# Kernel tuning notes

Hardware: AMD Instinct MI355X
Metric: run time of the kernel (lower is better)

## Reference

```python
import jax, jax.numpy as jnp
import numpy as np

N = 100000   # nodes
E = 1600000  # directed edges
F_IN = 100
H = 256
N_LABELS = 19
BN_EPS = 1e-5


def setup_inputs() -> dict:
    key = jax.random.key(0)
    ks = jax.random.split(key, 12)
    p = lambda k, shape, s=0.05: jax.random.normal(k, shape, dtype=jnp.float32) * s
    return {
        "x": jax.random.normal(ks[0], (N, F_IN), dtype=jnp.float32),
        "edge_index": jax.random.randint(ks[1], (2, E), 0, N, dtype=jnp.int32),
        "W1": p(ks[2], (F_IN, F_IN)), "b1": jnp.zeros((F_IN,), jnp.float32),
        "W2": p(ks[3], (F_IN, F_IN)), "b2": jnp.zeros((F_IN,), jnp.float32),
        "W3": p(ks[4], (F_IN, H)),   "b3": jnp.zeros((H,), jnp.float32),
        "fc1_W": p(ks[5], (H, H)),   "fc1_b": jnp.zeros((H,), jnp.float32),
        "fc2a_W": p(ks[6], (H, 128)), "fc2a_b": jnp.zeros((128,), jnp.float32),
        "bn_gamma": jnp.ones((128,), jnp.float32), "bn_beta": jnp.zeros((128,), jnp.float32),
        "fc2b_W": p(ks[7], (128, N_LABELS)), "fc2b_b": jnp.zeros((N_LABELS,), jnp.float32),
    }


def _gcn_conv(x, W, b, src, dst, dinv):
    """PyG GCNConv with add_self_loops + symmetric normalization.
    out[dst] += dinv[src]*dinv[dst] * (x @ W)[src], plus self-loop term, plus bias.
    """
    n = x.shape[0]
    xw = x @ W  # [N, out]
    norm = dinv[src] * dinv[dst]  # [E]
    agg = jax.ops.segment_sum(xw[src] * norm[:, None], dst, num_segments=n)
    agg = agg + xw * (dinv * dinv)[:, None]  # self loops (i -> i)
    return agg + b


def reference(x, edge_index, W1, b1, W2, b2, W3, b3, fc1_W, fc1_b,
              fc2a_W, fc2a_b, bn_gamma, bn_beta, fc2b_W, fc2b_b):
    src, dst = edge_index[0], edge_index[1]
    n = x.shape[0]
    # degree of augmented graph (A + I), computed on targets (sum aggregation)
    deg = jax.ops.segment_sum(jnp.ones((src.shape[0],), x.dtype), dst, num_segments=n) + 1.0
    dinv = jax.lax.rsqrt(deg)

    h = jnp.clip(x, -0.4, 0.4)
    h = jax.nn.relu(_gcn_conv(h, W1, b1, src, dst, dinv))
    h = jax.nn.relu(_gcn_conv(h, W2, b2, src, dst, dinv))
    h = jax.nn.relu(_gcn_conv(h, W3, b3, src, dst, dinv))
    h = jax.nn.relu(h @ fc1_W + fc1_b)
    # fc2: Linear -> BatchNorm1d (train mode, batch stats) -> ReLU -> Linear
    h = h @ fc2a_W + fc2a_b
    mu = jnp.mean(h, axis=0)
    var = jnp.mean(jnp.square(h - mu), axis=0)  # biased var, as torch BN uses
    h = (h - mu) * jax.lax.rsqrt(var + BN_EPS) * bn_gamma + bn_beta
    h = jax.nn.relu(h)
    logits = h @ fc2b_W + fc2b_b
    return jax.nn.log_softmax(logits, axis=1)
```

## Files before the change

kernel.cpp:

```cpp
#include <hip/hip_runtime.h>
#include <hip/hip_bf16.h>

#define N_NODES 100000
#define N_EDGES 1600000
#define F_IN_DIM 100
#define F_IN_PAD 104
#define H_DIM 256
#define BN_DIM 128
#define N_LABELS 19
#define BN_EPS 1e-5f
#define M_PAD 100096

#define BUCKET_SHIFT 8
#define NB 391
#define EPB 4096
#define PB 391

#define PACK_TOTAL 145728
#define CLIP_TOTAL (N_NODES * 13)

typedef __attribute__((ext_vector_type(8))) short bf16x8;
typedef __attribute__((ext_vector_type(4))) short s16x4;
typedef __attribute__((ext_vector_type(4))) float f32x4;

static __device__ inline short f2bf(float f) {
    __hip_bfloat16 h = __float2bfloat16(f);
    return *(short*)&h;
}
static __device__ inline float bf2f(short s) {
    unsigned u = ((unsigned)(unsigned short)s) << 16;
    return __builtin_bit_cast(float, u);
}

#define GLOAD_LDS16(g, l) \
    __builtin_amdgcn_global_load_lds((__attribute__((address_space(1))) const unsigned int*)(g), \
                                     (__attribute__((address_space(3))) unsigned int*)(l), 16, 0, 0)

__global__ __launch_bounds__(256) void part_hist_kernel(const int* __restrict__ dst,
                                                        int* __restrict__ part_hist, int E)
{
    __shared__ int h[NB];
    int tid = threadIdx.x;
    for (int i = tid; i < NB; i += 256) h[i] = 0;
    __syncthreads();
    int base = blockIdx.x * EPB;
    int end = min(base + EPB, E);
    for (int e = base + tid; e < end; e += 256)
        atomicAdd(&h[dst[e] >> BUCKET_SHIFT], 1);
    __syncthreads();
    for (int i = tid; i < NB; i += 256) part_hist[blockIdx.x * NB + i] = h[i];
}

__global__ __launch_bounds__(512) void bucket_total_kernel(const int* __restrict__ part_hist,
                                                           int* __restrict__ bucket_total)
{
    __shared__ int ls[512];
    int b = blockIdx.x;
    int s = 0;
    for (int p = threadIdx.x; p < PB; p += 512) s += part_hist[p * NB + b];
    ls[threadIdx.x] = s;
    __syncthreads();
    for (int off = 256; off > 0; off >>= 1) {
        if (threadIdx.x < off) ls[threadIdx.x] += ls[threadIdx.x + off];
        __syncthreads();
    }
    if (threadIdx.x == 0) bucket_total[b] = ls[0];
}

__global__ __launch_bounds__(512) void bucket_scan_kernel(const int* __restrict__ bucket_total,
                                                          int* __restrict__ bucket_base)
{
    __shared__ int ls[512];
    int tid = threadIdx.x;
    ls[tid] = (tid < NB) ? bucket_total[tid] : 0;
    __syncthreads();
    for (int off = 1; off < 512; off <<= 1) {
        int v = ls[tid];
        int add = (tid >= off) ? ls[tid - off] : 0;
        __syncthreads();
        ls[tid] = v + add;
        __syncthreads();
    }
    if (tid < NB) bucket_base[tid] = (tid > 0) ? ls[tid - 1] : 0;
    if (tid == 0) bucket_base[NB] = ls[NB - 1];
}

__global__ __launch_bounds__(512) void part_offset_kernel(int* __restrict__ part_hist,
                                                          const int* __restrict__ bucket_base)
{
    __shared__ int ls[512];
    int b = blockIdx.x;
    int tid = threadIdx.x;
    int v = (tid < PB) ? part_hist[tid * NB + b] : 0;
    ls[tid] = v;
    __syncthreads();
    for (int off = 1; off < 512; off <<= 1) {
        int x = ls[tid];
        int add = (tid >= off) ? ls[tid - off] : 0;
        __syncthreads();
        ls[tid] = x + add;
        __syncthreads();
    }
    if (tid < PB) part_hist[tid * NB + b] = bucket_base[b] + ((tid > 0) ? ls[tid - 1] : 0);
}

__global__ __launch_bounds__(256) void partition_kernel(const int* __restrict__ src,
                                                        const int* __restrict__ dst,
                                                        const int* __restrict__ part_hist,
                                                        int* __restrict__ ep, int E)
{
    __shared__ int cur[NB];
    int tid = threadIdx.x;
    for (int i = tid; i < NB; i += 256) cur[i] = part_hist[blockIdx.x * NB + i];
    __syncthreads();
    int base = blockIdx.x * EPB;
    int end = min(base + EPB, E);
    for (int e = base + tid; e < end; e += 256) {
        int d = dst[e];
        int s = src[e];
        int pos = atomicAdd(&cur[d >> BUCKET_SHIFT], 1);
        ep[pos] = (s << 8) | (d & 255);
    }
}

__global__ __launch_bounds__(256) void bucket_csr_kernel(const int* __restrict__ ep,
                                                         const int* __restrict__ bucket_base,
                                                         int* __restrict__ row_start,
                                                         float* __restrict__ dinv,
                                                         int* __restrict__ src_sorted, int N, int E)
{
    __shared__ int h[256], sc[256], cur[256];
    int b = blockIdx.x;
    int tid = threadIdx.x;
    int e0 = bucket_base[b], e1 = bucket_base[b + 1];
    int node0 = b << BUCKET_SHIFT;
    int nn = min(256, N - node0);

    h[tid] = 0;
    __syncthreads();
    for (int e = e0 + tid; e < e1; e += 256)
        atomicAdd(&h[ep[e] & 255], 1);
    __syncthreads();

    sc[tid] = h[tid];
    __syncthreads();
    for (int off = 1; off < 256; off <<= 1) {
        int v = sc[tid];
        int add = (tid >= off) ? sc[tid - off] : 0;
        __syncthreads();
        sc[tid] = v + add;
        __syncthreads();
    }
    int excl = e0 + ((tid > 0) ? sc[tid - 1] : 0);
    if (tid < nn) {
        row_start[node0 + tid] = excl;
        dinv[node0 + tid] = rsqrtf((float)h[tid] + 1.0f);
    }
    cur[tid] = excl;
    __syncthreads();
    for (int e = e0 + tid; e < e1; e += 256) {
        int p = ep[e];
        int pos = atomicAdd(&cur[p & 255], 1);
        src_sorted[pos] = ((unsigned)p) >> 8;
    }
    if (b == 0 && tid == 0) row_start[N] = E;
}

__global__ __launch_bounds__(256) void prep_kernel(
    const float* __restrict__ W1, const float* __restrict__ W2, const float* __restrict__ W3,
    const float* __restrict__ Wf1, const float* __restrict__ Wf2a, const float* __restrict__ x,
    short* __restrict__ Wt1, short* __restrict__ Wt2, short* __restrict__ Wt3,
    short* __restrict__ Wtf1, short* __restrict__ Wtf2a, short* __restrict__ xc)
{
    int idx = blockIdx.x * 256 + threadIdx.x;
    if (idx < PACK_TOTAL) {
        const float* W; short* Wt; int K, N, Kp, local;
        if (idx < 10400)       { W = W1;   Wt = Wt1;   K = 100; N = 100; Kp = 104; local = idx; }
        else if (idx < 20800)  { W = W2;   Wt = Wt2;   K = 100; N = 100; Kp = 104; local = idx - 10400; }
        else if (idx < 47424)  { W = W3;   Wt = Wt3;   K = 100; N = 256; Kp = 104; local = idx - 20800; }
        else if (idx < 112960) { W = Wf1;  Wt = Wtf1;  K = 256; N = 256; Kp = 256; local = idx - 47424; }
        else                   { W = Wf2a; Wt = Wtf2a; K = 256; N = 128; Kp = 256; local = idx - 112960; }
        int n = local / Kp, k = local - n * Kp;
        Wt[local] = (k < K) ? f2bf(W[(size_t)k * N + n]) : (short)0;
        return;
    }
    int cidx = idx - PACK_TOTAL;
    if (cidx >= CLIP_TOTAL) return;
    int r = cidx / 13, ch = cidx - r * 13;
    int c8 = ch * 8;
    const float* xr = x + (size_t)r * F_IN_DIM + c8;
    float v[8];
    float4 v0 = *(const float4*)(xr);
    v[0] = v0.x; v[1] = v0.y; v[2] = v0.z; v[3] = v0.w;
    if (c8 < 96) {
        float4 v1 = *(const float4*)(xr + 4);
        v[4] = v1.x; v[5] = v1.y; v[6] = v1.z; v[7] = v1.w;
    } else {
        v[4] = v[5] = v[6] = v[7] = 0.f;
    }
    bf16x8 o;
    #pragma unroll
    for (int j = 0; j < 8; j++)
        o[j] = f2bf(fminf(fmaxf(v[j], -0.4f), 0.4f));
    *(bf16x8*)(xc + (size_t)r * F_IN_PAD + c8) = o;
}

__global__ __launch_bounds__(256) void gemm_oneshot(
    const short* __restrict__ A,
    const short* __restrict__ Wt,
    const float* __restrict__ bias, const float* __restrict__ rowscale,
    short* __restrict__ C, int M, int Nout, int strideC, int relu)
{
    __shared__ __align__(16) short As[128 * F_IN_PAD];
    __shared__ __align__(16) short Bs[128 * F_IN_PAD];
    int tid = threadIdx.x;
    int wid = tid >> 6;
    int lane = tid & 63;
    int rowBase = blockIdx.x * 128;
    int colBase = blockIdx.y * 128;

    {
        const short* gb = (wid < 2) ? (A + (size_t)rowBase * F_IN_PAD)
                                    : (Wt + (size_t)colBase * F_IN_PAD);
        short* lb = (wid < 2) ? As : Bs;
        int half = (wid & 1) * 13;
        #pragma unroll
        for (int i = 0; i < 13; i++) {
            int c = half + i;
            GLOAD_LDS16(gb + c * 512 + lane * 8, lb + c * 512);
        }
    }
    __syncthreads();

    int quad = lane >> 4, l15 = lane & 15;
    int wave_m = (wid & 1) * 64;
    int wave_n = (wid >> 1) * 64;

    f32x4 acc[4][4];
    #pragma unroll
    for (int i = 0; i < 4; i++)
        #pragma unroll
        for (int j = 0; j < 4; j++)
            acc[i][j] = (f32x4){0.f, 0.f, 0.f, 0.f};

    #pragma unroll
    for (int kc = 0; kc < 4; kc++) {
        int off = kc * 32 + quad * 8;
        bool ok = (off + 8 <= F_IN_PAD);
        bf16x8 a[4], b[4];
        #pragma unroll
        for (int im = 0; im < 4; im++)
            a[im] = ok ? *(const bf16x8*)(As + (wave_m + im * 16 + l15) * F_IN_PAD + off)
                       : (bf16x8){0,0,0,0,0,0,0,0};
        #pragma unroll
        for (int in = 0; in < 4; in++)
            b[in] = ok ? *(const bf16x8*)(Bs + (wave_n + in * 16 + l15) * F_IN_PAD + off)
                       : (bf16x8){0,0,0,0,0,0,0,0};
        #pragma unroll
        for (int im = 0; im < 4; im++)
            #pragma unroll
            for (int in = 0; in < 4; in++)
                acc[im][in] = __builtin_amdgcn_mfma_f32_16x16x32_bf16(
                    a[im], b[in], acc[im][in], 0, 0, 0);
    }

    #pragma unroll
    for (int im = 0; im < 4; im++) {
        #pragma unroll
        for (int reg = 0; reg < 4; reg++) {
            int row = rowBase + wave_m + im * 16 + quad * 4 + reg;
            if (row >= M) continue;
            float rs = rowscale ? rowscale[row] : 1.f;
            #pragma unroll
            for (int in = 0; in < 4; in++) {
                int col = colBase + wave_n + in * 16 + l15;
                if (col >= strideC) continue;
                float v = 0.f;
                if (col < Nout) {
                    v = acc[im][in][reg];
                    if (bias) v += bias[col];
                    v *= rs;
                    if (relu) v = fmaxf(v, 0.f);
                }
                C[(size_t)row * strideC + col] = f2bf(v);
            }
        }
    }
}

__global__ __launch_bounds__(512, 4) void fc_fused_kernel(
    const short* __restrict__ A,
    const short* __restrict__ W1t,
    const float* __restrict__ b1v,
    const short* __restrict__ W2t,
    const float* __restrict__ b2v,
    short* __restrict__ C,
    float* __restrict__ bn_stats)
{
    __shared__ __align__(16) short SB[128 * 256];
    int tid = threadIdx.x;
    int wid = tid >> 6;
    int lane = tid & 63;
    int quad = lane >> 4, l15 = lane & 15;
    int rowBase = blockIdx.x * 128;
    int xr = (l15 & 7) << 4;

    if (blockIdx.x == 0 && tid < 256) bn_stats[tid] = 0.f;

    #pragma unroll
    for (int i = 0; i < 8; i++) {
        int c = i * 8 + wid;
        int r = c * 2 + (lane >> 5);
        int pb = ((lane & 31) * 16) ^ ((r & 7) << 4);
        const short* gp = A + (size_t)(rowBase + r) * H_DIM + (pb >> 1);
        GLOAD_LDS16(gp, SB + c * 512);
    }

    int wm = (wid & 1) * 64;
    int wn = (wid >> 1) * 64;

    f32x4 acc[4][4];
    #pragma unroll
    for (int i = 0; i < 4; i++)
        #pragma unroll
        for (int j = 0; j < 4; j++)
            acc[i][j] = (f32x4){0.f, 0.f, 0.f, 0.f};

    bf16x8 bA[4], bB[4];
    auto g1loadB = [&](bf16x8 (&dst)[4], int ks) {
        #pragma unroll
        for (int in = 0; in < 4; in++)
            dst[in] = *(const bf16x8*)(W1t + (size_t)(wn + in * 16 + l15) * H_DIM
                                       + ks * 32 + quad * 8);
    };
    auto g1step = [&](bf16x8 (&bc)[4], int ks) {
        bf16x8 a_[4];
        #pragma unroll
        for (int im = 0; im < 4; im++)
            a_[im] = *(const bf16x8*)(SB + (wm + im * 16 + l15) * 256
                                      + (((ks * 64 + quad * 16) ^ xr) >> 1));
        #pragma unroll
        for (int im = 0; im < 4; im++)
            #pragma unroll
            for (int in = 0; in < 4; in++)
                acc[im][in] = __builtin_amdgcn_mfma_f32_16x16x32_bf16(
                    bc[in], a_[im], acc[im][in], 0, 0, 0);
    };

    g1loadB(bA, 0);
    __syncthreads();

    g1loadB(bB, 1); g1step(bA, 0);
    g1loadB(bA, 2); g1step(bB, 1);
    g1loadB(bB, 3); g1step(bA, 2);
    g1loadB(bA, 4); g1step(bB, 3);
    g1loadB(bB, 5); g1step(bA, 4);
    g1loadB(bA, 6); g1step(bB, 5);
    g1loadB(bB, 7); g1step(bA, 6);
    g1step(bB, 7);

    float bb1[4][4];
    #pragma unroll
    for (int in = 0; in < 4; in++)
        #pragma unroll
        for (int r = 0; r < 4; r++)
            bb1[in][r] = b1v[wn + in * 16 + quad * 4 + r];

    __syncthreads();

    int wm2 = (wid & 1) * 64;
    int wn2 = (wid >> 1) * 32;
    bf16x8 cA[2], cB[2];
    auto g2loadB = [&](bf16x8 (&dst)[2], int ks) {
        #pragma unroll
        for (int in = 0; in < 2; in++)
            dst[in] = *(const bf16x8*)(W2t + (size_t)(wn2 + in * 16 + l15) * H_DIM
                                       + ks * 32 + quad * 8);
    };
    g2loadB(cA, 0);
    float bb2[2] = { b2v[wn2 + l15], b2v[wn2 + 16 + l15] };

    #pragma unroll
    for (int im = 0; im < 4; im++) {
        int ml = wm + im * 16 + l15;
        #pragma unroll
        for (int in = 0; in < 4; in++) {
            int nb = (wn + in * 16 + quad * 4) * 2;
            s16x4 o = (s16x4){
                f2bf(fmaxf(acc[im][in][0] + bb1[in][0], 0.f)),
                f2bf(fmaxf(acc[im][in][1] + bb1[in][1], 0.f)),
                f2bf(fmaxf(acc[im][in][2] + bb1[in][2], 0.f)),
                f2bf(fmaxf(acc[im][in][3] + bb1[in][3], 0.f))};
            *(s16x4*)(SB + ml * 256 + ((nb ^ xr) >> 1)) = o;
        }
    }
    __syncthreads();

    f32x4 acc2[4][2];
    #pragma unroll
    for (int i = 0; i < 4; i++)
        #pragma unroll
        for (int j = 0; j < 2; j++)
            acc2[i][j] = (f32x4){0.f, 0.f, 0.f, 0.f};

    auto g2step = [&](bf16x8 (&bc)[2], int ks) {
        bf16x8 a_[4];
        #pragma unroll
        for (int im = 0; im < 4; im++)
            a_[im] = *(const bf16x8*)(SB + (wm2 + im * 16 + l15) * 256
                                      + (((ks * 64 + quad * 16) ^ xr) >> 1));
        #pragma unroll
        for (int im = 0; im < 4; im++)
            #pragma unroll
            for (int in = 0; in < 2; in++)
                acc2[im][in] = __builtin_amdgcn_mfma_f32_16x16x32_bf16(
                    a_[im], bc[in], acc2[im][in], 0, 0, 0);
    };

    g2loadB(cB, 1); g2step(cA, 0);
    g2loadB(cA, 2); g2step(cB, 1);
    g2loadB(cB, 3); g2step(cA, 2);
    g2loadB(cA, 4); g2step(cB, 3);
    g2loadB(cB, 5); g2step(cA, 4);
    g2loadB(cA, 6); g2step(cB, 5);
    g2loadB(cB, 7); g2step(cA, 6);
    g2step(cB, 7);

    #pragma unroll
    for (int im = 0; im < 4; im++) {
        #pragma unroll
        for (int reg = 0; reg < 4; reg++) {
            int row = rowBase + wm2 + im * 16 + quad * 4 + reg;
            #pragma unroll
            for (int in = 0; in < 2; in++) {
                int col = wn2 + in * 16 + l15;
                C[(size_t)row * BN_DIM + col] = f2bf(acc2[im][in][reg] + bb2[in]);
            }
        }
    }
}

template<int F, int STRIDE, int T, int MODE>
__global__ void gather_kernel(const short* __restrict__ xws,
                              const int* __restrict__ row_start,
                              const int* __restrict__ src_sorted,
                              const float* __restrict__ dinv,
                              const float* __restrict__ bias,
                              short* __restrict__ out, int n)
{
    constexpr int CHUNKS = STRIDE / 8;
    int group = (blockIdx.x * blockDim.x + threadIdx.x) / T;
    int lane = threadIdx.x % T;
    if (group >= n || lane >= CHUNKS) return;
    int d = group;
    int e0 = row_start[d], e1 = row_start[d + 1];
    int coff = lane * 8;
    const short* base = xws + coff;

    float acc[8] = {}, acc2[8] = {};
    int e = e0;
    for (; e + 3 < e1; e += 4) {
        int s0 = src_sorted[e + 0];
        int s1 = src_sorted[e + 1];
        int s2 = src_sorted[e + 2];
        int s3 = src_sorted[e + 3];
        bf16x8 v0 = *(const bf16x8*)(base + (size_t)s0 * STRIDE);
        bf16x8 v1 = *(const bf16x8*)(base + (size_t)s1 * STRIDE);
        bf16x8 v2 = *(const bf16x8*)(base + (size_t)s2 * STRIDE);
        bf16x8 v3 = *(const bf16x8*)(base + (size_t)s3 * STRIDE);
        #pragma unroll
        for (int j = 0; j < 8; j++) {
            acc[j]  += bf2f(v0[j]) + bf2f(v2[j]);
            acc2[j] += bf2f(v1[j]) + bf2f(v3[j]);
        }
    }
    for (; e < e1; e++) {
        int s = src_sorted[e];
        bf16x8 v = *(const bf16x8*)(base + (size_t)s * STRIDE);
        #pragma unroll
        for (int j = 0; j < 8; j++) acc[j] += bf2f(v[j]);
    }

    bf16x8 xv = *(const bf16x8*)(xws + (size_t)d * STRIDE + coff);
    float di = dinv[d];
    bf16x8 o;
    #pragma unroll
    for (int j = 0; j < 8; j++) {
        int col = coff + j;
        float v = 0.f;
        if (col < F) {
            v = di * (acc[j] + acc2[j] + bf2f(xv[j]));
            if (MODE == 0) v = fmaxf(v + bias[col], 0.f);
            if (MODE == 1) v = di * fmaxf(v + bias[col], 0.f);
        }
        o[j] = f2bf(v);
    }
    *(bf16x8*)(out + (size_t)d * STRIDE + coff) = o;
}

__global__ void bn_stats_kernel(const short* __restrict__ h,
                                float* __restrict__ sum, float* __restrict__ sumsq, int Ntot)
{
    int c = threadIdx.x & 127;
    int rpb = blockDim.x >> 7;
    int r0 = blockIdx.x * rpb + (threadIdx.x >> 7);
    int stride = gridDim.x * rpb;
    float s = 0.f, ss = 0.f;
    for (int r = r0; r < Ntot; r += stride) {
        float v = bf2f(h[(size_t)r * BN_DIM + c]);
        s += v; ss += v * v;
    }
    __shared__ float ls[256], lss[256];
    ls[threadIdx.x] = s; lss[threadIdx.x] = ss;
    __syncthreads();
    if (threadIdx.x < 128) {
        s = ls[threadIdx.x] + ls[threadIdx.x + 128];
        ss = lss[threadIdx.x] + lss[threadIdx.x + 128];
        atomicAdd(&sum[c], s);
        atomicAdd(&sumsq[c], ss);
    }
}

__global__ __launch_bounds__(256) void fc2b_fused_kernel(
    const short* __restrict__ h, const float* __restrict__ bn_sum, const float* __restrict__ bn_sumsq,
    const float* __restrict__ gamma, const float* __restrict__ beta,
    const float* __restrict__ W, const float* __restrict__ bias,
    float* __restrict__ out, int Ntot)
{
    __shared__ float Ws[BN_DIM][N_LABELS + 1];
    __shared__ float as[BN_DIM], bs[BN_DIM];
    for (int i = threadIdx.x; i < BN_DIM * N_LABELS; i += 256) {
        int k = i / N_LABELS, j = i - k * N_LABELS;
        Ws[k][j] = W[i];
    }
    if (threadIdx.x < BN_DIM) {
        int c = threadIdx.x;
        float inv_n = 1.0f / (float)Ntot;
        float mu = bn_sum[c] * inv_n;
        float var = bn_sumsq[c] * inv_n - mu * mu;
        float ai = gamma[c] * rsqrtf(var + BN_EPS);
        as[c] = ai;
        bs[c] = beta[c] - mu * ai;
    }
    __syncthreads();

    int r = blockIdx.x * 256 + threadIdx.x;
    if (r >= Ntot) return;

    float acc[N_LABELS];
    #pragma unroll
    for (int j = 0; j < N_LABELS; j++) acc[j] = bias[j];

    const short* hr = h + (size_t)r * BN_DIM;
    #pragma unroll
    for (int k0 = 0; k0 < BN_DIM; k0 += 8) {
        bf16x8 hv = *(const bf16x8*)(hr + k0);
        #pragma unroll
        for (int t = 0; t < 8; t++) {
            float v = fmaxf(bf2f(hv[t]) * as[k0 + t] + bs[k0 + t], 0.f);
            #pragma unroll
            for (int j = 0; j < N_LABELS; j++)
                acc[j] = fmaf(v, Ws[k0 + t][j], acc[j]);
        }
    }

    float m = acc[0];
    #pragma unroll
    for (int j = 1; j < N_LABELS; j++) m = fmaxf(m, acc[j]);
    float s = 0.f;
    #pragma unroll
    for (int j = 0; j < N_LABELS; j++) s += expf(acc[j] - m);
    float lse = m + logf(s);
    float* o = out + (size_t)r * N_LABELS;
    #pragma unroll
    for (int j = 0; j < N_LABELS; j++) o[j] = acc[j] - lse;
}

extern "C" void kernel_launch(void* const* d_in, const int* in_sizes, int n_in,
                              void* d_out, int out_size, void* d_ws, size_t ws_size,
                              hipStream_t stream)
{
    const float* x      = (const float*)d_in[0];
    const int*   ei     = (const int*)d_in[1];
    const float* W1     = (const float*)d_in[2];
    const float* b1     = (const float*)d_in[3];
    const float* W2     = (const float*)d_in[4];
    const float* b2     = (const float*)d_in[5];
    const float* W3     = (const float*)d_in[6];
    const float* b3     = (const float*)d_in[7];
    const float* fc1_W  = (const float*)d_in[8];
    const float* fc1_b  = (const float*)d_in[9];
    const float* fc2aW  = (const float*)d_in[10];
    const float* fc2ab  = (const float*)d_in[11];
    const float* gamma  = (const float*)d_in[12];
    const float* beta   = (const float*)d_in[13];
    const float* fc2bW  = (const float*)d_in[14];
    const float* fc2bb  = (const float*)d_in[15];
    float* out = (float*)d_out;

    const int* src = ei;
    const int* dst = ei + N_EDGES;

    char* w = (char*)d_ws;
    float* dinv        = (float*)w;  w += ((size_t)N_NODES * 4 + 255) / 256 * 256;
    int*   row_start   = (int*)w;    w += ((size_t)(N_NODES + 1) * 4 + 255) / 256 * 256;
    int*   part_hist   = (int*)w;    w += ((size_t)PB * NB * 4 + 255) / 256 * 256;
    int*   bucket_total= (int*)w;    w += ((size_t)NB * 4 + 255) / 256 * 256;
    int*   bucket_base = (int*)w;    w += ((size_t)(NB + 1) * 4 + 255) / 256 * 256;
    float* bn_sum      = (float*)w;  w += 128 * 4;
    float* bn_sumsq    = (float*)w;  w += 128 * 4;
    short* Wt1         = (short*)w;  w += ((size_t)F_IN_DIM * F_IN_PAD * 2 + 255) / 256 * 256;
    short* Wt2         = (short*)w;  w += ((size_t)F_IN_DIM * F_IN_PAD * 2 + 255) / 256 * 256;
    short* Wt3         = (short*)w;  w += ((size_t)H_DIM * F_IN_PAD * 2 + 255) / 256 * 256;
    short* Wtf1        = (short*)w;  w += ((size_t)H_DIM * H_DIM * 2 + 255) / 256 * 256;
    short* Wtf2a       = (short*)w;  w += ((size_t)BN_DIM * H_DIM * 2 + 255) / 256 * 256;
    int*   src_sorted  = (int*)w;    w += ((size_t)N_EDGES * 4 + 255) / 256 * 256;
    int*   ep          = (int*)w;    w += ((size_t)N_EDGES * 4 + 255) / 256 * 256;
    short* xws100      = (short*)w;  w += ((size_t)M_PAD * F_IN_PAD * 2 + 255) / 256 * 256;
    short* agg100      = (short*)w;  w += ((size_t)M_PAD * F_IN_PAD * 2 + 255) / 256 * 256;
    short* big1        = (short*)w;  w += ((size_t)M_PAD * H_DIM * 2 + 255) / 256 * 256;
    short* big2        = (short*)w;  w += ((size_t)M_PAD * H_DIM * 2 + 255) / 256 * 256;

    short* xclip = big1;

    part_hist_kernel<<<PB, 256, 0, stream>>>(dst, part_hist, N_EDGES);
    bucket_total_kernel<<<NB, 512, 0, stream>>>(part_hist, bucket_total);
    bucket_scan_kernel<<<1, 512, 0, stream>>>(bucket_total, bucket_base);
    part_offset_kernel<<<NB, 512, 0, stream>>>(part_hist, bucket_base);
    partition_kernel<<<PB, 256, 0, stream>>>(src, dst, part_hist, ep, N_EDGES);
    bucket_csr_kernel<<<NB, 256, 0, stream>>>(ep, bucket_base, row_start, dinv,
                                              src_sorted, N_NODES, N_EDGES);

    prep_kernel<<<(PACK_TOTAL + CLIP_TOTAL + 255) / 256, 256, 0, stream>>>(
        W1, W2, W3, fc1_W, fc2aW, x, Wt1, Wt2, Wt3, Wtf1, Wtf2a, xclip);

    const int nOne = (N_NODES + 127) / 128;
    int gatherBlocks = (N_NODES * 16 + 255) / 256;

    gemm_oneshot<<<dim3(nOne, 1), 256, 0, stream>>>(
        xclip, Wt1, nullptr, dinv, xws100, N_NODES, F_IN_DIM, F_IN_PAD, 0);
    gather_kernel<F_IN_DIM, F_IN_PAD, 16, 0><<<gatherBlocks, 256, 0, stream>>>(
        xws100, row_start, src_sorted, dinv, b1, agg100, N_NODES);

    gemm_oneshot<<<dim3(nOne, 1), 256, 0, stream>>>(
        agg100, Wt2, nullptr, dinv, xws100, N_NODES, F_IN_DIM, F_IN_PAD, 0);
    gather_kernel<F_IN_DIM, F_IN_PAD, 16, 1><<<gatherBlocks, 256, 0, stream>>>(
        xws100, row_start, src_sorted, dinv, b2, agg100, N_NODES);

    gather_kernel<F_IN_DIM, F_IN_PAD, 16, 2><<<gatherBlocks, 256, 0, stream>>>(
        agg100, row_start, src_sorted, dinv, nullptr, xws100, N_NODES);
    gemm_oneshot<<<dim3(nOne, 2), 256, 0, stream>>>(
        xws100, Wt3, b3, nullptr, big1, N_NODES, H_DIM, H_DIM, 1);

    fc_fused_kernel<<<nOne, 512, 0, stream>>>(
        big1, Wtf1, fc1_b, Wtf2a, fc2ab, big2, bn_sum);

    bn_stats_kernel<<<512, 256, 0, stream>>>(big2, bn_sum, bn_sumsq, N_NODES);

    fc2b_fused_kernel<<<(N_NODES + 255) / 256, 256, 0, stream>>>(
        big2, bn_sum, bn_sumsq, gamma, beta, fc2bW, fc2bb, out, N_NODES);
}
```

Baseline: 596.5 us.

## Pad features to 128, swizzle GEMM LDS, slice gather by column blocks

Widens the padded feature stride from 104 to 128 so each row is 256 bytes, and adds an XOR swizzle to the LDS tile loads and fragment reads in the one-shot GEMM to avoid bank conflicts. The gather kernel is reorganised so each block covers 128 destination nodes for one 16-column slice, two threads per node, so all blocks share one slice of the feature table in cache. Index loads and output stores are marked nontemporal. The cost is more bytes per row (including padding columns) and more redundant reads of the CSR offsets and indices, one set per slice.

```diff
diff --git a/kernel.cpp b/kernel.cpp
--- a/kernel.cpp
+++ b/kernel.cpp
@@ -4,7 +4,7 @@
 #define N_NODES 100000
 #define N_EDGES 1600000
 #define F_IN_DIM 100
-#define F_IN_PAD 104
+#define F_IN_PAD 128
 #define H_DIM 256
 #define BN_DIM 128
 #define N_LABELS 19
@@ -16,8 +16,8 @@
 #define EPB 4096
 #define PB 391
 
-#define PACK_TOTAL 145728
-#define CLIP_TOTAL (N_NODES * 13)
+#define PACK_TOTAL 156672
+#define CLIP_TOTAL (N_NODES * 16)
 
 typedef __attribute__((ext_vector_type(8))) short bf16x8;
 typedef __attribute__((ext_vector_type(4))) short s16x4;
@@ -175,28 +175,28 @@
     int idx = blockIdx.x * 256 + threadIdx.x;
     if (idx < PACK_TOTAL) {
         const float* W; short* Wt; int K, N, Kp, local;
-        if (idx < 10400)       { W = W1;   Wt = Wt1;   K = 100; N = 100; Kp = 104; local = idx; }
-        else if (idx < 20800)  { W = W2;   Wt = Wt2;   K = 100; N = 100; Kp = 104; local = idx - 10400; }
-        else if (idx < 47424)  { W = W3;   Wt = Wt3;   K = 100; N = 256; Kp = 104; local = idx - 20800; }
-        else if (idx < 112960) { W = Wf1;  Wt = Wtf1;  K = 256; N = 256; Kp = 256; local = idx - 47424; }
-        else                   { W = Wf2a; Wt = Wtf2a; K = 256; N = 128; Kp = 256; local = idx - 112960; }
+        if (idx < 12800)       { W = W1;   Wt = Wt1;   K = 100; N = 100; Kp = 128; local = idx; }
+        else if (idx < 25600)  { W = W2;   Wt = Wt2;   K = 100; N = 100; Kp = 128; local = idx - 12800; }
+        else if (idx < 58368)  { W = W3;   Wt = Wt3;   K = 100; N = 256; Kp = 128; local = idx - 25600; }
+        else if (idx < 123904) { W = Wf1;  Wt = Wtf1;  K = 256; N = 256; Kp = 256; local = idx - 58368; }
+        else                   { W = Wf2a; Wt = Wtf2a; K = 256; N = 128; Kp = 256; local = idx - 123904; }
         int n = local / Kp, k = local - n * Kp;
         Wt[local] = (k < K) ? f2bf(W[(size_t)k * N + n]) : (short)0;
         return;
     }
     int cidx = idx - PACK_TOTAL;
     if (cidx >= CLIP_TOTAL) return;
-    int r = cidx / 13, ch = cidx - r * 13;
+    int r = cidx >> 4, ch = cidx & 15;
     int c8 = ch * 8;
-    const float* xr = x + (size_t)r * F_IN_DIM + c8;
-    float v[8];
-    float4 v0 = *(const float4*)(xr);
-    v[0] = v0.x; v[1] = v0.y; v[2] = v0.z; v[3] = v0.w;
-    if (c8 < 96) {
-        float4 v1 = *(const float4*)(xr + 4);
-        v[4] = v1.x; v[5] = v1.y; v[6] = v1.z; v[7] = v1.w;
-    } else {
-        v[4] = v[5] = v[6] = v[7] = 0.f;
+    float v[8] = {0.f, 0.f, 0.f, 0.f, 0.f, 0.f, 0.f, 0.f};
+    if (c8 < 100) {
+        const float* xr = x + (size_t)r * F_IN_DIM + c8;
+        float4 v0 = *(const float4*)(xr);
+        v[0] = v0.x; v[1] = v0.y; v[2] = v0.z; v[3] = v0.w;
+        if (c8 < 96) {
+            float4 v1 = *(const float4*)(xr + 4);
+            v[4] = v1.x; v[5] = v1.y; v[6] = v1.z; v[7] = v1.w;
+        }
     }
     bf16x8 o;
     #pragma unroll
@@ -223,16 +223,19 @@
         const short* gb = (wid < 2) ? (A + (size_t)rowBase * F_IN_PAD)
                                     : (Wt + (size_t)colBase * F_IN_PAD);
         short* lb = (wid < 2) ? As : Bs;
-        int half = (wid & 1) * 13;
-        #pragma unroll
-        for (int i = 0; i < 13; i++) {
+        int half = (wid & 1) * 16;
+        #pragma unroll
+        for (int i = 0; i < 16; i++) {
             int c = half + i;
-            GLOAD_LDS16(gb + c * 512 + lane * 8, lb + c * 512);
+            int r = c * 4 + (lane >> 4);
+            int pb = ((lane & 15) * 16) ^ ((r & 7) << 4);
+            GLOAD_LDS16(gb + r * F_IN_PAD + (pb >> 1), lb + c * 512);
         }
     }
     __syncthreads();
 
     int quad = lane >> 4, l15 = lane & 15;
+    int xr = (l15 & 7) << 4;
     int wave_m = (wid & 1) * 64;
     int wave_n = (wid >> 1) * 64;
 
@@ -245,17 +248,16 @@
 
     #pragma unroll
     for (int kc = 0; kc < 4; kc++) {
-        int off = kc * 32 + quad * 8;
-        bool ok = (off + 8 <= F_IN_PAD);
+        int ob = kc * 64 + quad * 16;
         bf16x8 a[4], b[4];
         #pragma unroll
         for (int im = 0; im < 4; im++)
-            a[im] = ok ? *(const bf16x8*)(As + (wave_m + im * 16 + l15) * F_IN_PAD + off)
-                       : (bf16x8){0,0,0,0,0,0,0,0};
+            a[im] = *(const bf16x8*)(As + (wave_m + im * 16 + l15) * F_IN_PAD
+                                     + ((ob ^ xr) >> 1));
         #pragma unroll
         for (int in = 0; in < 4; in++)
-            b[in] = ok ? *(const bf16x8*)(Bs + (wave_n + in * 16 + l15) * F_IN_PAD + off)
-                       : (bf16x8){0,0,0,0,0,0,0,0};
+            b[in] = *(const bf16x8*)(Bs + (wave_n + in * 16 + l15) * F_IN_PAD
+                                     + ((ob ^ xr) >> 1));
         #pragma unroll
         for (int im = 0; im < 4; im++)
             #pragma unroll
@@ -440,7 +442,7 @@
     }
 }
 
-template<int F, int STRIDE, int T, int MODE>
+template<int F, int MODE>
 __global__ void gather_kernel(const short* __restrict__ xws,
                               const int* __restrict__ row_start,
                               const int* __restrict__ src_sorted,
@@ -448,26 +450,26 @@
                               const float* __restrict__ bias,
                               short* __restrict__ out, int n)
 {
-    constexpr int CHUNKS = STRIDE / 8;
-    int group = (blockIdx.x * blockDim.x + threadIdx.x) / T;
-    int lane = threadIdx.x % T;
-    if (group >= n || lane >= CHUNKS) return;
-    int d = group;
-    int e0 = row_start[d], e1 = row_start[d + 1];
-    int coff = lane * 8;
+    int slice = blockIdx.x & 7;
+    int lane = threadIdx.x & 1;
+    int d = (blockIdx.x >> 3) * 128 + (threadIdx.x >> 1);
+    if (d >= n) return;
+    int e0 = __builtin_nontemporal_load(row_start + d);
+    int e1 = __builtin_nontemporal_load(row_start + d + 1);
+    int coff = slice * 16 + lane * 8;
     const short* base = xws + coff;
 
     float acc[8] = {}, acc2[8] = {};
     int e = e0;
     for (; e + 3 < e1; e += 4) {
-        int s0 = src_sorted[e + 0];
-        int s1 = src_sorted[e + 1];
-        int s2 = src_sorted[e + 2];
-        int s3 = src_sorted[e + 3];
-        bf16x8 v0 = *(const bf16x8*)(base + (size_t)s0 * STRIDE);
-        bf16x8 v1 = *(const bf16x8*)(base + (size_t)s1 * STRIDE);
-        bf16x8 v2 = *(const bf16x8*)(base + (size_t)s2 * STRIDE);
-        bf16x8 v3 = *(const bf16x8*)(base + (size_t)s3 * STRIDE);
+        int s0 = __builtin_nontemporal_load(src_sorted + e + 0);
+        int s1 = __builtin_nontemporal_load(src_sorted + e + 1);
+        int s2 = __builtin_nontemporal_load(src_sorted + e + 2);
+        int s3 = __builtin_nontemporal_load(src_sorted + e + 3);
+        bf16x8 v0 = *(const bf16x8*)(base + (size_t)s0 * F_IN_PAD);
+        bf16x8 v1 = *(const bf16x8*)(base + (size_t)s1 * F_IN_PAD);
+        bf16x8 v2 = *(const bf16x8*)(base + (size_t)s2 * F_IN_PAD);
+        bf16x8 v3 = *(const bf16x8*)(base + (size_t)s3 * F_IN_PAD);
         #pragma unroll
         for (int j = 0; j < 8; j++) {
             acc[j]  += bf2f(v0[j]) + bf2f(v2[j]);
@@ -475,13 +477,13 @@
         }
     }
     for (; e < e1; e++) {
-        int s = src_sorted[e];
-        bf16x8 v = *(const bf16x8*)(base + (size_t)s * STRIDE);
+        int s = __builtin_nontemporal_load(src_sorted + e);
+        bf16x8 v = *(const bf16x8*)(base + (size_t)s * F_IN_PAD);
         #pragma unroll
         for (int j = 0; j < 8; j++) acc[j] += bf2f(v[j]);
     }
 
-    bf16x8 xv = *(const bf16x8*)(xws + (size_t)d * STRIDE + coff);
+    bf16x8 xv = *(const bf16x8*)(base + (size_t)d * F_IN_PAD);
     float di = dinv[d];
     bf16x8 o;
     #pragma unroll
@@ -495,7 +497,7 @@
         }
         o[j] = f2bf(v);
     }
-    *(bf16x8*)(out + (size_t)d * STRIDE + coff) = o;
+    __builtin_nontemporal_store(o, (bf16x8*)(out + (size_t)d * F_IN_PAD + coff));
 }
 
 __global__ void bn_stats_kernel(const short* __restrict__ h,
@@ -635,19 +637,19 @@
         W1, W2, W3, fc1_W, fc2aW, x, Wt1, Wt2, Wt3, Wtf1, Wtf2a, xclip);
 
     const int nOne = (N_NODES + 127) / 128;
-    int gatherBlocks = (N_NODES * 16 + 255) / 256;
+    const int gatherGrid = nOne * 8;
 
     gemm_oneshot<<<dim3(nOne, 1), 256, 0, stream>>>(
         xclip, Wt1, nullptr, dinv, xws100, N_NODES, F_IN_DIM, F_IN_PAD, 0);
-    gather_kernel<F_IN_DIM, F_IN_PAD, 16, 0><<<gatherBlocks, 256, 0, stream>>>(
+    gather_kernel<F_IN_DIM, 0><<<gatherGrid, 256, 0, stream>>>(
         xws100, row_start, src_sorted, dinv, b1, agg100, N_NODES);
 
     gemm_oneshot<<<dim3(nOne, 1), 256, 0, stream>>>(
         agg100, Wt2, nullptr, dinv, xws100, N_NODES, F_IN_DIM, F_IN_PAD, 0);
-    gather_kernel<F_IN_DIM, F_IN_PAD, 16, 1><<<gatherBlocks, 256, 0, stream>>>(
+    gather_kernel<F_IN_DIM, 1><<<gatherGrid, 256, 0, stream>>>(
         xws100, row_start, src_sorted, dinv, b2, agg100, N_NODES);
 
-    gather_kernel<F_IN_DIM, F_IN_PAD, 16, 2><<<gatherBlocks, 256, 0, stream>>>(
+    gather_kernel<F_IN_DIM, 2><<<gatherGrid, 256, 0, stream>>>(
         agg100, row_start, src_sorted, dinv, nullptr, xws100, N_NODES);
     gemm_oneshot<<<dim3(nOne, 2), 256, 0, stream>>>(
         xws100, Wt3, b3, nullptr, big1, N_NODES, H_DIM, H_DIM, 1);
```

New measurement: 1.085 ms. +82.0%, slower.
